# Performance work log

Hardware: AMD Instinct MI355X
Metric: run time of the kernel (lower is better)

## Reference

```python
import jax, jax.numpy as jnp
import numpy as np

THRESHOLD = 1.0
CURRENT_DECAY = 0.5
VOLTAGE_DECAY = 0.5
WEIGHT_SCALE = 2.0  # slayer block weight_scale=2, weight_norm=False


def spike_fn(v):
    # Heaviside spike with hard threshold (forward only)
    return (v >= THRESHOLD).astype(v.dtype)


def conv_transpose_2d(x, w):
    # x: [NT, Cin, H, W]; w: [Cin, Cout, k, k] (pytorch ConvTranspose2d layout)
    # Equivalent dilated conv: swap in/out, flip spatial taps.
    rhs = jnp.transpose(w, (1, 0, 2, 3))[:, :, ::-1, ::-1]
    return jax.lax.conv_general_dilated(
        x, rhs, window_strides=(1, 1), padding=[(1, 1), (1, 1)],
        lhs_dilation=(2, 2), dimension_numbers=('NCHW', 'OIHW', 'NCHW'))


def cuba_block(x, w):
    # x: [N, Cin, H, W, T] -> spikes [N, Cout, 2H-1, 2W-1, T]
    N, Cin, H, W, T = x.shape
    xt = jnp.transpose(x, (4, 0, 1, 2, 3)).reshape(T * N, Cin, H, W)
    z = conv_transpose_2d(xt, WEIGHT_SCALE * w)  # synapse over all timesteps at once
    Cout, Ho, Wo = z.shape[1], z.shape[2], z.shape[3]
    z = z.reshape(T, N, Cout, Ho, Wo)

    def step(carry, zt):
        cur, vol = carry
        cur = (1.0 - CURRENT_DECAY) * cur + zt          # CUBA current dynamics
        vol = (1.0 - VOLTAGE_DECAY) * vol + cur          # CUBA voltage dynamics
        s = spike_fn(vol)
        vol = vol * (1.0 - s)                            # reset voltage on spike
        return (cur, vol), s

    init = (jnp.zeros_like(z[0]), jnp.zeros_like(z[0]))
    _, spikes = jax.lax.scan(step, init, z)              # [T, N, Cout, Ho, Wo]
    return jnp.transpose(spikes, (1, 2, 3, 4, 0))


def setup_inputs() -> dict:
    key = jax.random.key(0)
    k1, k2, k3, k4 = jax.random.split(key, 4)
    c_hid, C = 32, 2
    spike = (jax.random.uniform(k1, (4, c_hid * 4, 16, 16, 32)) < 0.3).astype(jnp.float32)

    def winit(k, cin, cout):
        return jax.random.normal(k, (cin, cout, 3, 3), jnp.float32) / np.sqrt(cin * 9.0)

    return {
        'spike': spike,
        'w1': winit(k2, c_hid * 4, c_hid * 2),
        'w2': winit(k3, c_hid * 2, c_hid),
        'w3': winit(k4, c_hid, C),
    }


def reference(spike, w1, w2, w3):
    counts = []
    for w in (w1, w2, w3):
        spike = cuba_block(spike, w)
        counts.append(jnp.mean(spike))
    return spike, jnp.stack(counts).reshape(1, -1)
```

## Files before the change

kernel.cpp:

```cpp
#include <hip/hip_runtime.h>

#define TT 32

__device__ __forceinline__ float bf16_bits_to_f32(unsigned short u) {
    unsigned v = ((unsigned)u) << 16; float f; __builtin_memcpy(&f, &v, 4); return f;
}
__device__ __forceinline__ unsigned short f32_to_bf16_rne(float f) {
    unsigned u; __builtin_memcpy(&u, &f, 4);
    u += 0x7FFFu + ((u >> 16) & 1u);
    return (unsigned short)(u >> 16);
}
__device__ __forceinline__ float round_bf16_f32(float f) {
    return bf16_bits_to_f32(f32_to_bf16_rne(f));
}
__device__ __forceinline__ float f64_to_bf16_f32(double d) {
    float fz = __double2float_rz(d);
    if ((double)fz != d) {
        unsigned u; __builtin_memcpy(&u, &fz, 4); u |= 1u; __builtin_memcpy(&fz, &u, 4);
    }
    return round_bf16_f32(fz);
}
__device__ __forceinline__ unsigned spread4(unsigned b) {
    unsigned x = (b | (b << 12)) & 0x000F000Fu;
    x = (x | (x << 6)) & 0x03030303u;
    x = (x | (x << 3)) & 0x11111111u;
    return x;
}

__global__ void detect_and_init(const unsigned* __restrict__ spk,
                                int* __restrict__ flag, float* __restrict__ sums)
{
    unsigned w = spk[threadIdx.x];
    bool ok = (w == 0u) || (w == 0x3F800000u);
    unsigned long long vote = __ballot(ok);
    if (threadIdx.x == 0) {
        flag[0] = (vote == 0xFFFFFFFFFFFFFFFFull) ? 0 : 1;
        sums[0] = 0.f; sums[1] = 0.f; sums[2] = 0.f;
    }
}

__global__ __launch_bounds__(256)
void pack_interleave(const void* __restrict__ ginv, unsigned* __restrict__ idx0,
                     const int* __restrict__ flag)
{
    const int gid = blockIdx.x * 256 + threadIdx.x;
    if (gid >= 32768) return;
    const int site = gid & 255;
    const int g    = (gid >> 8) & 31;
    const int n    = gid >> 13;

    unsigned m[4];
    #pragma unroll
    for (int k = 0; k < 4; ++k) {
        const size_t ebase = ((size_t)(n * 128 + 4 * g + k) * 256 + site) * TT;
        unsigned mask = 0u;
        if (flag[0]) {
            const uint4* p = (const uint4*)((const unsigned short*)ginv + ebase);
            #pragma unroll
            for (int q = 0; q < 4; ++q) {
                uint4 a = p[q];
                unsigned wd[4] = {a.x, a.y, a.z, a.w};
                #pragma unroll
                for (int mm = 0; mm < 4; ++mm) {
                    const int t = q * 8 + mm * 2;
                    mask |= (wd[mm] & 0xFFFFu) ? (1u << t)       : 0u;
                    mask |= (wd[mm] >> 16)     ? (1u << (t + 1)) : 0u;
                }
            }
        } else {
            const float4* p = (const float4*)((const float*)ginv + ebase);
            #pragma unroll
            for (int j = 0; j < 8; ++j) {
                float4 v = p[j];
                mask |= (v.x != 0.f) ? (1u << (j * 4 + 0)) : 0u;
                mask |= (v.y != 0.f) ? (1u << (j * 4 + 1)) : 0u;
                mask |= (v.z != 0.f) ? (1u << (j * 4 + 2)) : 0u;
                mask |= (v.w != 0.f) ? (1u << (j * 4 + 3)) : 0u;
            }
        }
        m[k] = mask;
    }
    #pragma unroll
    for (int q = 0; q < 4; ++q) {
        const unsigned w =  spread4((m[0] >> (8 * q)) & 0xFFu)
                         | (spread4((m[1] >> (8 * q)) & 0xFFu) << 1)
                         | (spread4((m[2] >> (8 * q)) & 0xFFu) << 2)
                         | (spread4((m[3] >> (8 * q)) & 0xFFu) << 3);
        idx0[q * 32768 + gid] = w;
    }
}

template<int C, int PLANE>
__global__ __launch_bounds__(256)
void pack_mid(const unsigned* __restrict__ masks, unsigned* __restrict__ idx)
{
    constexpr int G = C / 4;
    constexpr int TOT = 4 * G * PLANE;
    const int gid = blockIdx.x * 256 + threadIdx.x;
    if (gid >= TOT) return;
    const int site = gid % PLANE;
    const int g    = (gid / PLANE) % G;
    const int n    = gid / (PLANE * G);
    unsigned m[4];
    #pragma unroll
    for (int k = 0; k < 4; ++k)
        m[k] = masks[(n * C + 4 * g + k) * PLANE + site];
    #pragma unroll
    for (int q = 0; q < 4; ++q) {
        const unsigned w =  spread4((m[0] >> (8 * q)) & 0xFFu)
                         | (spread4((m[1] >> (8 * q)) & 0xFFu) << 1)
                         | (spread4((m[2] >> (8 * q)) & 0xFFu) << 2)
                         | (spread4((m[3] >> (8 * q)) & 0xFFu) << 3);
        idx[q * TOT + gid] = w;
    }
}

template<int CIN, int COUT, bool LAST>
__global__ __launch_bounds__(256, 4)
void cuba_layer(const unsigned* __restrict__ idxIn, const void* __restrict__ wptr,
                void* __restrict__ goutv, unsigned* __restrict__ maskOut,
                int N, int Hi, int Wi, float* __restrict__ sumOut,
                const int* __restrict__ flag)
{
    constexpr int G = CIN / 4;
    const bool isbf = (flag[0] != 0);
    const int Ho = 2 * Hi - 1, Wo = 2 * Wi - 1;
    const int co = (int)blockIdx.y;
    const int zz = 3 - (int)blockIdx.z;
    const int po = zz >> 1, pw = zz & 1;
    const int lg = po + pw;
    const int nTap = 1 << lg;
    const int nH = Hi - po, nW = Wi - pw;
    const int sites = N * nH * nW;
    const int siteBase = (int)blockIdx.x * 256;
    if (siteBase >= sites) return;

    __shared__ double lut[G][4][16];
    {
        const unsigned short* w16 = (const unsigned short*)wptr;
        const float* w32 = (const float*)wptr;
        const int entries = G * nTap * 16;
        for (int e = threadIdx.x; e < entries; e += 256) {
            const int idx = e & 15;
            const int tp  = (e >> 4) & (nTap - 1);
            const int g   = e >> (4 + lg);
            const int v = (po && (tp >= (pw ? 2 : 1))) ? 1 : 0;
            const int h = pw ? (tp & 1) : 0;
            const int kh = v ? 0 : (po ? 2 : 1);
            const int kw = h ? 0 : (pw ? 2 : 1);
            const int wof = kh * 3 + kw;
            double s = 0.0;
            #pragma unroll
            for (int k = 0; k < 4; ++k) {
                if ((idx >> k) & 1) {
                    const int wi = ((4 * g + k) * COUT + co) * 9 + wof;
                    const float wraw = isbf ? bf16_bits_to_f32(w16[wi]) : w32[wi];
                    s += 2.0 * (double)wraw;
                }
            }
            lut[g][tp][idx] = s;
        }
    }
    __syncthreads();

    const int siteIdx = siteBase + (int)threadIdx.x;
    float cnt = 0.f;

    if (siteIdx < sites) {
        const int b  = siteIdx % nW;
        const int t1 = siteIdx / nW;
        const int a  = t1 % nH;
        const int n  = t1 / nH;
        const int oh = 2 * a + po, ow = 2 * b + pw;
        const int plane = Hi * Wi;
        const int QT = N * G * plane;

        const int siteA = a * Wi + b;
        const int siteB = siteA + 1;
        const int siteC = siteA + Wi;
        const int siteD = siteC + 1;

        unsigned mask = 0u;
        float  curF = 0.f, volF = 0.f;
        double curD = 0.0, volD = 0.0;

        #pragma unroll 1
        for (int p = 0; p < 4; ++p) {
            double acc[8];
            #pragma unroll
            for (int j = 0; j < 8; ++j) acc[j] = 0.0;

            const unsigned* pb = idxIn + (size_t)p * QT + (size_t)(n * G) * plane;
            for (int g = 0; g < G; ++g) {
                const unsigned* bp = pb + (size_t)g * plane;
                {
                    const unsigned w = bp[siteA];
                    #pragma unroll
                    for (int j = 0; j < 8; ++j)
                        acc[j] += lut[g][0][(w >> (4 * j)) & 0xFu];
                }
                if (pw) {
                    const unsigned w = bp[siteB];
                    #pragma unroll
                    for (int j = 0; j < 8; ++j)
                        acc[j] += lut[g][1][(w >> (4 * j)) & 0xFu];
                }
                if (po) {
                    const unsigned w = bp[siteC];
                    #pragma unroll
                    for (int j = 0; j < 8; ++j)
                        acc[j] += lut[g][pw ? 2 : 1][(w >> (4 * j)) & 0xFu];
                }
                if (po && pw) {
                    const unsigned w = bp[siteD];
                    #pragma unroll
                    for (int j = 0; j < 8; ++j)
                        acc[j] += lut[g][3][(w >> (4 * j)) & 0xFu];
                }
            }

            if (isbf) {
                #pragma unroll
                for (int j = 0; j < 8; ++j) {
                    const int t = p * 8 + j;
                    const float z = f64_to_bf16_f32(acc[j]);
                    curF = round_bf16_f32(0.5f * curF + z);
                    volF = round_bf16_f32(0.5f * volF + curF);
                    const bool fire = (volF >= 1.0f);
                    mask |= fire ? (1u << t) : 0u;
                    volF = fire ? 0.f : volF;
                }
            } else {
                #pragma unroll
                for (int j = 0; j < 8; ++j) {
                    const int t = p * 8 + j;
                    curD = fma(0.5, curD, acc[j]);
                    volD = fma(0.5, volD, curD);
                    const bool fire = (volD >= 1.0);
                    mask |= fire ? (1u << t) : 0u;
                    volD = fire ? 0.0 : volD;
                }
            }
        }
        cnt = (float)__popc(mask);

        const int gidOut = ((n * COUT + co) * Ho + oh) * Wo + ow;
        if (LAST) {
            if (isbf) {
                uint4* ob = (uint4*)((unsigned short*)goutv + (size_t)gidOut * TT);
                #pragma unroll
                for (int q = 0; q < 4; ++q) {
                    unsigned wd[4];
                    #pragma unroll
                    for (int m2 = 0; m2 < 4; ++m2) {
                        const int t = (q * 4 + m2) * 2;
                        wd[m2] = (((mask >> t) & 1u) ? 0x3F80u : 0u)
                               | (((mask >> (t + 1)) & 1u) ? 0x3F800000u : 0u);
                    }
                    ob[q] = make_uint4(wd[0], wd[1], wd[2], wd[3]);
                }
            } else {
                float4* ob = (float4*)((float*)goutv + (size_t)gidOut * TT);
                #pragma unroll
                for (int j = 0; j < 8; ++j) {
                    float4 s4;
                    s4.x = (mask >> (j * 4 + 0)) & 1u ? 1.0f : 0.0f;
                    s4.y = (mask >> (j * 4 + 1)) & 1u ? 1.0f : 0.0f;
                    s4.z = (mask >> (j * 4 + 2)) & 1u ? 1.0f : 0.0f;
                    s4.w = (mask >> (j * 4 + 3)) & 1u ? 1.0f : 0.0f;
                    ob[j] = s4;
                }
            }
        } else {
            maskOut[gidOut] = mask;
        }
    }

    #pragma unroll
    for (int o = 32; o >= 1; o >>= 1) cnt += __shfl_down(cnt, o);
    if ((threadIdx.x & 63) == 0 && cnt > 0.f) atomicAdd(sumOut, cnt);
}

__global__ void finalize_counts(const float* __restrict__ sums,
                                void* __restrict__ out, const int* __restrict__ flag)
{
    int i = threadIdx.x;
    if (i < 3) {
        const float numel[3] = {7872512.f, 15239168.f, 3748096.f};
        float v = sums[i] / numel[i];
        if (flag[0]) ((unsigned short*)out)[3748096 + i] = f32_to_bf16_rne(v);
        else         ((float*)out)[3748096 + i] = v;
    }
}

extern "C" void kernel_launch(void* const* d_in, const int* in_sizes, int n_in,
                              void* d_out, int out_size, void* d_ws, size_t ws_size,
                              hipStream_t stream)
{
    const void* x  = d_in[0];
    const void* w1 = d_in[1];
    const void* w2 = d_in[2];
    const void* w3 = d_in[3];

    unsigned* bufA = (unsigned*)d_ws;
    unsigned* bufB = bufA + 476288;
    unsigned* idx0 = bufB;
    float* sums = (float*)(bufB + 476288);
    int*   flag = (int*)(sums + 3);

    detect_and_init<<<1, 64, 0, stream>>>((const unsigned*)x, flag, sums);
    pack_interleave<<<128, 256, 0, stream>>>(x, idx0, flag);

    cuba_layer<128, 64, false><<<dim3(4, 64, 4), 256, 0, stream>>>(
        idx0, w1, nullptr, bufA, 4, 16, 16, sums + 0, flag);
    pack_mid<64, 961><<<241, 256, 0, stream>>>(bufA, bufB);
    cuba_layer<64, 32, false><<<dim3(16, 32, 4), 256, 0, stream>>>(
        bufB, w2, nullptr, bufA, 4, 31, 31, sums + 1, flag);
    pack_mid<32, 3721><<<466, 256, 0, stream>>>(bufA, bufB);
    cuba_layer<32, 2, true><<<dim3(59, 2, 4), 256, 0, stream>>>(
        bufB, w3, d_out, nullptr, 4, 61, 61, sums + 2, flag);

    finalize_counts<<<1, 64, 0, stream>>>(sums, d_out, flag);
}
```

Baseline: 393.0 us.

## Split conv taps across thread slabs with shared-memory reduction to balance parity classes

The tap accumulation for each output site is spread across several thread slabs, so that blocks handling the 4-tap parity class use more threads per site and finish in about the same time as the 1-tap blocks. Partial sums are exchanged through a shared double buffer and reduced by slab 0, which then runs the CUBA recurrence. Grid sizes grow to cover the smaller number of sites per block. The cost is extra barriers, shared-memory traffic and idle threads in slab 0 during the recurrence, plus lower occupancy from the larger shared allocation.

New measurement: 423.6 us. 7.8% more time.

```diff
diff --git a/kernel.cpp b/kernel.cpp
--- a/kernel.cpp
+++ b/kernel.cpp
@@ -115,7 +115,7 @@
     }
 }
 
-template<int CIN, int COUT, bool LAST>
+template<int CIN, int COUT, int MODE, bool LAST>
 __global__ __launch_bounds__(256, 4)
 void cuba_layer(const unsigned* __restrict__ idxIn, const void* __restrict__ wptr,
                 void* __restrict__ goutv, unsigned* __restrict__ maskOut,
@@ -123,6 +123,7 @@
                 const int* __restrict__ flag)
 {
     constexpr int G = CIN / 4;
+    constexpr int XW = (MODE == 1) ? 1536 : 1024;
     const bool isbf = (flag[0] != 0);
     const int Ho = 2 * Hi - 1, Wo = 2 * Wi - 1;
     const int co = (int)blockIdx.y;
@@ -132,10 +133,14 @@
     const int nTap = 1 << lg;
     const int nH = Hi - po, nW = Wi - pw;
     const int sites = N * nH * nW;
-    const int siteBase = (int)blockIdx.x * 256;
+    const int lS = (MODE == 1) ? lg : ((zz == 3) ? 1 : 0);
+    const int S  = 1 << lS;
+    const int spb = 256 >> lS;
+    const int siteBase = (int)blockIdx.x * spb;
     if (siteBase >= sites) return;
 
     __shared__ double lut[G][4][16];
+    __shared__ double xch[XW];
     {
         const unsigned short* w16 = (const unsigned short*)wptr;
         const float* w32 = (const float*)wptr;
@@ -163,62 +168,86 @@
     }
     __syncthreads();
 
-    const int siteIdx = siteBase + (int)threadIdx.x;
+    const int slab = (int)threadIdx.x >> (8 - lS);
+    const int sl   = (int)threadIdx.x & (spb - 1);
+    const int siteIdx = siteBase + sl;
+    const bool valid = siteIdx < sites;
+    const int sIdx = valid ? siteIdx : 0;
+
+    const int b  = sIdx % nW;
+    const int t1v = sIdx / nW;
+    const int a  = t1v % nH;
+    const int n  = t1v / nH;
+    const int oh = 2 * a + po, ow = 2 * b + pw;
+    const int plane = Hi * Wi;
+    const int QT = N * G * plane;
+
+    const int siteA = a * Wi + b;
+    const int siteB = siteA + 1;
+    const int siteC = siteA + Wi;
+    const int siteD = siteC + 1;
+
+    int s1 = siteA, tp1 = 0, s2 = 0, tp2 = 0;
+    bool two = false;
+    if (MODE == 0) {
+        if (zz == 3) {
+            if (slab == 0) { s1 = siteA; tp1 = 0; s2 = siteB; tp2 = 1; two = true; }
+            else           { s1 = siteC; tp1 = 2; s2 = siteD; tp2 = 3; two = true; }
+        } else if (zz == 1) { s2 = siteB; tp2 = 1; two = true; }
+        else if (zz == 2)   { s2 = siteC; tp2 = 1; two = true; }
+    } else {
+        if (zz == 1)      { if (slab == 1) { s1 = siteB; tp1 = 1; } }
+        else if (zz == 2) { if (slab == 1) { s1 = siteC; tp1 = 1; } }
+        else if (zz == 3) {
+            if      (slab == 1) { s1 = siteB; tp1 = 1; }
+            else if (slab == 2) { s1 = siteC; tp1 = 2; }
+            else if (slab == 3) { s1 = siteD; tp1 = 3; }
+        }
+    }
+
+    unsigned mask = 0u;
+    float  curF = 0.f, volF = 0.f;
+    double curD = 0.0, volD = 0.0;
     float cnt = 0.f;
 
-    if (siteIdx < sites) {
-        const int b  = siteIdx % nW;
-        const int t1 = siteIdx / nW;
-        const int a  = t1 % nH;
-        const int n  = t1 / nH;
-        const int oh = 2 * a + po, ow = 2 * b + pw;
-        const int plane = Hi * Wi;
-        const int QT = N * G * plane;
-
-        const int siteA = a * Wi + b;
-        const int siteB = siteA + 1;
-        const int siteC = siteA + Wi;
-        const int siteD = siteC + 1;
-
-        unsigned mask = 0u;
-        float  curF = 0.f, volF = 0.f;
-        double curD = 0.0, volD = 0.0;
-
-        #pragma unroll 1
-        for (int p = 0; p < 4; ++p) {
-            double acc[8];
+    #pragma unroll 1
+    for (int p = 0; p < 4; ++p) {
+        double acc[8];
+        #pragma unroll
+        for (int j = 0; j < 8; ++j) acc[j] = 0.0;
+
+        const unsigned* pb = idxIn + (size_t)p * QT + (size_t)(n * G) * plane;
+        #pragma unroll 4
+        for (int g = 0; g < G; ++g) {
+            const unsigned* bp = pb + (size_t)g * plane;
+            const unsigned w1 = bp[s1];
             #pragma unroll
-            for (int j = 0; j < 8; ++j) acc[j] = 0.0;
-
-            const unsigned* pb = idxIn + (size_t)p * QT + (size_t)(n * G) * plane;
-            for (int g = 0; g < G; ++g) {
-                const unsigned* bp = pb + (size_t)g * plane;
-                {
-                    const unsigned w = bp[siteA];
+            for (int j = 0; j < 8; ++j)
+                acc[j] += lut[g][tp1][(w1 >> (4 * j)) & 0xFu];
+            if (two) {
+                const unsigned w2 = bp[s2];
+                #pragma unroll
+                for (int j = 0; j < 8; ++j)
+                    acc[j] += lut[g][tp2][(w2 >> (4 * j)) & 0xFu];
+            }
+        }
+
+        if (S > 1) {
+            if (slab != 0) {
+                #pragma unroll
+                for (int j = 0; j < 8; ++j)
+                    xch[(slab - 1) * (8 * spb) + j * spb + sl] = acc[j];
+            }
+            __syncthreads();
+            if (slab == 0) {
+                for (int s = 1; s < S; ++s)
                     #pragma unroll
                     for (int j = 0; j < 8; ++j)
-                        acc[j] += lut[g][0][(w >> (4 * j)) & 0xFu];
-                }
-                if (pw) {
-                    const unsigned w = bp[siteB];
-                    #pragma unroll
-                    for (int j = 0; j < 8; ++j)
-                        acc[j] += lut[g][1][(w >> (4 * j)) & 0xFu];
-                }
-                if (po) {
-                    const unsigned w = bp[siteC];
-                    #pragma unroll
-                    for (int j = 0; j < 8; ++j)
-                        acc[j] += lut[g][pw ? 2 : 1][(w >> (4 * j)) & 0xFu];
-                }
-                if (po && pw) {
-                    const unsigned w = bp[siteD];
-                    #pragma unroll
-                    for (int j = 0; j < 8; ++j)
-                        acc[j] += lut[g][3][(w >> (4 * j)) & 0xFu];
-                }
-            }
-
+                        acc[j] += xch[(s - 1) * (8 * spb) + j * spb + sl];
+            }
+        }
+
+        if (slab == 0) {
             if (isbf) {
                 #pragma unroll
                 for (int j = 0; j < 8; ++j) {
@@ -242,8 +271,11 @@
                 }
             }
         }
+        if (S > 1) __syncthreads();
+    }
+
+    if (slab == 0 && valid) {
         cnt = (float)__popc(mask);
-
         const int gidOut = ((n * COUT + co) * Ho + oh) * Wo + ow;
         if (LAST) {
             if (isbf) {
@@ -311,13 +343,13 @@
     detect_and_init<<<1, 64, 0, stream>>>((const unsigned*)x, flag, sums);
     pack_interleave<<<128, 256, 0, stream>>>(x, idx0, flag);
 
-    cuba_layer<128, 64, false><<<dim3(4, 64, 4), 256, 0, stream>>>(
+    cuba_layer<128, 64, 0, false><<<dim3(8, 64, 4), 256, 0, stream>>>(
         idx0, w1, nullptr, bufA, 4, 16, 16, sums + 0, flag);
     pack_mid<64, 961><<<241, 256, 0, stream>>>(bufA, bufB);
-    cuba_layer<64, 32, false><<<dim3(16, 32, 4), 256, 0, stream>>>(
+    cuba_layer<64, 32, 0, false><<<dim3(29, 32, 4), 256, 0, stream>>>(
         bufB, w2, nullptr, bufA, 4, 31, 31, sums + 1, flag);
     pack_mid<32, 3721><<<466, 256, 0, stream>>>(bufA, bufB);
-    cuba_layer<32, 2, true><<<dim3(59, 2, 4), 256, 0, stream>>>(
+    cuba_layer<32, 2, 1, true><<<dim3(225, 2, 4), 256, 0, stream>>>(
         bufB, w3, d_out, nullptr, 4, 61, 61, sums + 2, flag);
 
     finalize_counts<<<1, 64, 0, stream>>>(sums, d_out, flag);
```

## Interleave packed timestep quarters and accumulate all 32 timesteps in one pass

Applied to the files above, without the earlier changes.

The packed spike index now stores the four 8-timestep quarters of each site contiguously as one uint4 instead of in four separate planes. The layer kernel reads each site once with a 128-bit load and accumulates all 32 timesteps in one loop over channel groups. Previously it looped over the four quarters and re-walked the channel groups each time. This removes three of the four passes over the LUT loop and the index reads, but holds 32 double accumulators per thread. The launch-bounds occupancy hint is dropped to make room for that register pressure, which may lower occupancy.

After: 438.7 us. 11.6% more time.

```diff
diff --git a/kernel.cpp b/kernel.cpp
--- a/kernel.cpp
+++ b/kernel.cpp
@@ -80,14 +80,14 @@
         }
         m[k] = mask;
     }
-    #pragma unroll
-    for (int q = 0; q < 4; ++q) {
-        const unsigned w =  spread4((m[0] >> (8 * q)) & 0xFFu)
-                         | (spread4((m[1] >> (8 * q)) & 0xFFu) << 1)
-                         | (spread4((m[2] >> (8 * q)) & 0xFFu) << 2)
-                         | (spread4((m[3] >> (8 * q)) & 0xFFu) << 3);
-        idx0[q * 32768 + gid] = w;
-    }
+    unsigned w[4];
+    #pragma unroll
+    for (int q = 0; q < 4; ++q)
+        w[q] =  spread4((m[0] >> (8 * q)) & 0xFFu)
+             | (spread4((m[1] >> (8 * q)) & 0xFFu) << 1)
+             | (spread4((m[2] >> (8 * q)) & 0xFFu) << 2)
+             | (spread4((m[3] >> (8 * q)) & 0xFFu) << 3);
+    *(uint4*)(idx0 + (size_t)gid * 4) = make_uint4(w[0], w[1], w[2], w[3]);
 }
 
 template<int C, int PLANE>
@@ -105,18 +105,18 @@
     #pragma unroll
     for (int k = 0; k < 4; ++k)
         m[k] = masks[(n * C + 4 * g + k) * PLANE + site];
-    #pragma unroll
-    for (int q = 0; q < 4; ++q) {
-        const unsigned w =  spread4((m[0] >> (8 * q)) & 0xFFu)
-                         | (spread4((m[1] >> (8 * q)) & 0xFFu) << 1)
-                         | (spread4((m[2] >> (8 * q)) & 0xFFu) << 2)
-                         | (spread4((m[3] >> (8 * q)) & 0xFFu) << 3);
-        idx[q * TOT + gid] = w;
-    }
+    unsigned w[4];
+    #pragma unroll
+    for (int q = 0; q < 4; ++q)
+        w[q] =  spread4((m[0] >> (8 * q)) & 0xFFu)
+             | (spread4((m[1] >> (8 * q)) & 0xFFu) << 1)
+             | (spread4((m[2] >> (8 * q)) & 0xFFu) << 2)
+             | (spread4((m[3] >> (8 * q)) & 0xFFu) << 3);
+    *(uint4*)(idx + (size_t)gid * 4) = make_uint4(w[0], w[1], w[2], w[3]);
 }
 
 template<int CIN, int COUT, bool LAST>
-__global__ __launch_bounds__(256, 4)
+__global__ __launch_bounds__(256)
 void cuba_layer(const unsigned* __restrict__ idxIn, const void* __restrict__ wptr,
                 void* __restrict__ goutv, unsigned* __restrict__ maskOut,
                 int N, int Hi, int Wi, float* __restrict__ sumOut,
@@ -173,73 +173,79 @@
         const int n  = t1 / nH;
         const int oh = 2 * a + po, ow = 2 * b + pw;
         const int plane = Hi * Wi;
-        const int QT = N * G * plane;
 
         const int siteA = a * Wi + b;
         const int siteB = siteA + 1;
         const int siteC = siteA + Wi;
         const int siteD = siteC + 1;
 
+        double acc[TT];
+        #pragma unroll
+        for (int t = 0; t < TT; ++t) acc[t] = 0.0;
+
+        for (int g = 0; g < G; ++g) {
+            const unsigned* bp = idxIn + (size_t)(n * G + g) * plane * 4;
+
+            {
+                const uint4 w4 = *(const uint4*)(bp + (size_t)siteA * 4);
+                const unsigned wd[4] = {w4.x, w4.y, w4.z, w4.w};
+                #pragma unroll
+                for (int q = 0; q < 4; ++q)
+                    #pragma unroll
+                    for (int j = 0; j < 8; ++j)
+                        acc[q * 8 + j] += lut[g][0][(wd[q] >> (4 * j)) & 0xFu];
+            }
+            if (pw) {
+                const uint4 w4 = *(const uint4*)(bp + (size_t)siteB * 4);
+                const unsigned wd[4] = {w4.x, w4.y, w4.z, w4.w};
+                #pragma unroll
+                for (int q = 0; q < 4; ++q)
+                    #pragma unroll
+                    for (int j = 0; j < 8; ++j)
+                        acc[q * 8 + j] += lut[g][1][(wd[q] >> (4 * j)) & 0xFu];
+            }
+            if (po) {
+                const int tp = pw ? 2 : 1;
+                const uint4 w4 = *(const uint4*)(bp + (size_t)siteC * 4);
+                const unsigned wd[4] = {w4.x, w4.y, w4.z, w4.w};
+                #pragma unroll
+                for (int q = 0; q < 4; ++q)
+                    #pragma unroll
+                    for (int j = 0; j < 8; ++j)
+                        acc[q * 8 + j] += lut[g][tp][(wd[q] >> (4 * j)) & 0xFu];
+            }
+            if (po && pw) {
+                const uint4 w4 = *(const uint4*)(bp + (size_t)siteD * 4);
+                const unsigned wd[4] = {w4.x, w4.y, w4.z, w4.w};
+                #pragma unroll
+                for (int q = 0; q < 4; ++q)
+                    #pragma unroll
+                    for (int j = 0; j < 8; ++j)
+                        acc[q * 8 + j] += lut[g][3][(wd[q] >> (4 * j)) & 0xFu];
+            }
+        }
+
         unsigned mask = 0u;
-        float  curF = 0.f, volF = 0.f;
-        double curD = 0.0, volD = 0.0;
-
-        #pragma unroll 1
-        for (int p = 0; p < 4; ++p) {
-            double acc[8];
-            #pragma unroll
-            for (int j = 0; j < 8; ++j) acc[j] = 0.0;
-
-            const unsigned* pb = idxIn + (size_t)p * QT + (size_t)(n * G) * plane;
-            for (int g = 0; g < G; ++g) {
-                const unsigned* bp = pb + (size_t)g * plane;
-                {
-                    const unsigned w = bp[siteA];
-                    #pragma unroll
-                    for (int j = 0; j < 8; ++j)
-                        acc[j] += lut[g][0][(w >> (4 * j)) & 0xFu];
-                }
-                if (pw) {
-                    const unsigned w = bp[siteB];
-                    #pragma unroll
-                    for (int j = 0; j < 8; ++j)
-                        acc[j] += lut[g][1][(w >> (4 * j)) & 0xFu];
-                }
-                if (po) {
-                    const unsigned w = bp[siteC];
-                    #pragma unroll
-                    for (int j = 0; j < 8; ++j)
-                        acc[j] += lut[g][pw ? 2 : 1][(w >> (4 * j)) & 0xFu];
-                }
-                if (po && pw) {
-                    const unsigned w = bp[siteD];
-                    #pragma unroll
-                    for (int j = 0; j < 8; ++j)
-                        acc[j] += lut[g][3][(w >> (4 * j)) & 0xFu];
-                }
-            }
-
-            if (isbf) {
-                #pragma unroll
-                for (int j = 0; j < 8; ++j) {
-                    const int t = p * 8 + j;
-                    const float z = f64_to_bf16_f32(acc[j]);
-                    curF = round_bf16_f32(0.5f * curF + z);
-                    volF = round_bf16_f32(0.5f * volF + curF);
-                    const bool fire = (volF >= 1.0f);
-                    mask |= fire ? (1u << t) : 0u;
-                    volF = fire ? 0.f : volF;
-                }
-            } else {
-                #pragma unroll
-                for (int j = 0; j < 8; ++j) {
-                    const int t = p * 8 + j;
-                    curD = fma(0.5, curD, acc[j]);
-                    volD = fma(0.5, volD, curD);
-                    const bool fire = (volD >= 1.0);
-                    mask |= fire ? (1u << t) : 0u;
-                    volD = fire ? 0.0 : volD;
-                }
+        if (isbf) {
+            float cur = 0.f, vol = 0.f;
+            #pragma unroll
+            for (int t = 0; t < TT; ++t) {
+                const float z = f64_to_bf16_f32(acc[t]);
+                cur = round_bf16_f32(0.5f * cur + z);
+                vol = round_bf16_f32(0.5f * vol + cur);
+                const bool fire = (vol >= 1.0f);
+                mask |= fire ? (1u << t) : 0u;
+                vol = fire ? 0.f : vol;
+            }
+        } else {
+            double cur = 0.0, vol = 0.0;
+            #pragma unroll
+            for (int t = 0; t < TT; ++t) {
+                cur = fma(0.5, cur, acc[t]);
+                vol = fma(0.5, vol, cur);
+                const bool fire = (vol >= 1.0);
+                mask |= fire ? (1u << t) : 0u;
+                vol = fire ? 0.0 : vol;
             }
         }
         cnt = (float)__popc(mask);
```
